# Performance work log

Hardware: AMD Instinct MI355X
Metric: run time of the kernel (lower is better)

The kernel has to match this reference:

```python
import jax, jax.numpy as jnp
from jax import lax
import numpy as np

STRIDE = 16
PRE_NMS = 100        # pre_nms_topN hardcoded in original forward
NMS_THRESH = 0.3
MIN_SIZE = 8.0


def _mk(ws, hs, xc, yc):
    return np.stack([xc - 0.5 * (ws - 1), yc - 0.5 * (hs - 1),
                     xc + 0.5 * (ws - 1), yc + 0.5 * (hs - 1)], axis=1)


def _generate_anchors(base_size=16, ratios=(0.5, 1.0, 2.0), scales=(8, 16, 32)):
    ratios = np.asarray(ratios, np.float64)
    scales = np.asarray(scales, np.float64)
    xc = yc = 0.5 * (base_size - 1)
    size = float(base_size) * float(base_size)
    ws = np.round(np.sqrt(size / ratios))
    hs = np.round(ws * ratios)
    ratio_anchors = _mk(ws, hs, xc, yc)
    out = []
    for a in ratio_anchors:
        aw = a[2] - a[0] + 1.0
        ah = a[3] - a[1] + 1.0
        axc = a[0] + 0.5 * (aw - 1)
        ayc = a[1] + 0.5 * (ah - 1)
        out.append(_mk(aw * scales, ah * scales, axc, ayc))
    return np.concatenate(out, axis=0)

ANCHORS = jnp.asarray(_generate_anchors(16, (0.5, 1.0, 2.0), (8, 16, 32)), jnp.float32)  # [9,4]
A = ANCHORS.shape[0]


def setup_inputs() -> dict:
    key = jax.random.key(0)
    k1, k2 = jax.random.split(key)
    B, H, W = 32, 80, 120
    score = jax.random.normal(k1, (B, 2 * A, H, W), jnp.float32)
    delta = jax.random.normal(k2, (B, 4 * A, H, W), jnp.float32)
    img = jnp.array([H * STRIDE, W * STRIDE, 1.0], jnp.float32)  # (im_h, im_w, scale)
    return {"score": score, "delta": delta, "img": img}


def _nms_one(bx, sv, vd):
    # bx: [P,4] boxes sorted by score, sv: [P] scores, vd: [P] valid mask
    b = lax.stop_gradient(bx)  # NMS selection is non-differentiable (index-based)
    x1, y1, x2, y2 = b[:, 0], b[:, 1], b[:, 2], b[:, 3]
    area = (x2 - x1 + 1.0) * (y2 - y1 + 1.0)
    iw = jnp.clip(jnp.minimum(x2[:, None], x2[None, :]) - jnp.maximum(x1[:, None], x1[None, :]) + 1.0, 0.0)
    ih = jnp.clip(jnp.minimum(y2[:, None], y2[None, :]) - jnp.maximum(y1[:, None], y1[None, :]) + 1.0, 0.0)
    inter = iw * ih
    iou = inter / (area[:, None] + area[None, :] - inter)  # [P,P]
    idx = jnp.arange(PRE_NMS)

    def body(i, keep):
        sup = (iou[i] > NMS_THRESH) & (idx > i) & keep[i]
        return keep & ~sup

    keep = lax.fori_loop(0, PRE_NMS, body, vd)
    # compact kept rows to the front, zeros after (matches original's zero-padded output)
    pos = jnp.cumsum(keep) - 1
    dst = jnp.where(keep, pos, PRE_NMS)  # dropped rows go to scratch row
    rows = jnp.concatenate([bx, sv[:, None]], axis=1)  # [P,5]
    return jnp.zeros((PRE_NMS + 1, 5), bx.dtype).at[dst].set(rows)[:PRE_NMS]


def reference(score, delta, img):
    B, _, h, w = delta.shape
    # objectness scores: second half of channels, laid out (h, w, A)
    scores = score[:, A:, :, :].transpose(0, 2, 3, 1).reshape(B, -1)  # [B, h*w*A]
    # shifts enumerated j over h (outer), i over w (inner)
    sx, sy = jnp.meshgrid(jnp.arange(w) * STRIDE, jnp.arange(h) * STRIDE)  # [h,w]
    shifts = jnp.stack([sx.ravel(), sy.ravel(), sx.ravel(), sy.ravel()], axis=1).astype(score.dtype)
    anchors = (ANCHORS[None, :, :] + shifts[:, None, :]).reshape(-1, 4)  # [h*w*A, 4]
    # NOTE: original assigns deltas = delta.view(B,-1,4), discarding the permute (bug kept)
    deltas = delta.reshape(B, -1, 4)
    # bbox_transform_inv
    aw = anchors[:, 2] - anchors[:, 0] + 1.0
    ah = anchors[:, 3] - anchors[:, 1] + 1.0
    acx = anchors[:, 0] + 0.5 * aw
    acy = anchors[:, 1] + 0.5 * ah
    pcx = deltas[:, :, 0] * aw + acx
    pcy = deltas[:, :, 1] * ah + acy
    pw = jnp.exp(deltas[:, :, 2]) * aw
    ph = jnp.exp(deltas[:, :, 3]) * ah
    x1 = pcx - 0.5 * pw
    y1 = pcy - 0.5 * ph
    x2 = pcx + 0.5 * pw
    y2 = pcy + 0.5 * ph
    # clip_boxes to image: x in [0, im_w-1], y in [0, im_h-1]
    x1 = jnp.clip(x1, 0.0, img[1] - 1.0)
    x2 = jnp.clip(x2, 0.0, img[1] - 1.0)
    y1 = jnp.clip(y1, 0.0, img[0] - 1.0)
    y2 = jnp.clip(y2, 0.0, img[0] - 1.0)
    proposals = jnp.stack([x1, y1, x2, y2], axis=-1)  # [B,N,4]
    # _filter_boxes with keep[0] applied to ALL images (bug in original, kept)
    ws_ = x2 - x1 + 1.0
    hs_ = y2 - y1 + 1.0
    keep0 = (ws_[0] >= MIN_SIZE) & (hs_[0] >= MIN_SIZE)  # [N]
    scores = jnp.where(keep0[None, :], scores, -jnp.inf)  # filtered boxes sort last
    topv, topi = lax.top_k(scores, PRE_NMS)  # [B,P]
    boxes = jnp.take_along_axis(proposals, topi[:, :, None], axis=1)  # [B,P,4]
    valid = jnp.isfinite(topv)
    return jax.vmap(_nms_one)(boxes, topv, valid)  # [B,P,5]
```

## Files before the change

### kernel.cpp

```cpp
#include <hip/hip_runtime.h>
#include <math.h>

#define NA     9
#define HH     80
#define WWID   120
#define HWSZ   (HH * WWID)
#define NANC   (HWSZ * NA)
#define NANC4  (NANC / 4)
#define PRE_NMS 100
#define NMS_THRESH 0.3f
#define MIN_SIZE 8.0f
#define STRIDE_F 16.0f
#define NCH    22
#define SLOTS  46
#define NFAST  (NCH * SLOTS)
#define NBIN   4096
#define CAPF   2048
#define T0ORD  0xC0300000u

__constant__ float c_aw[NA] = {184.f, 368.f, 736.f, 128.f, 256.f, 512.f,  88.f, 176.f, 352.f};
__constant__ float c_ah[NA] = { 96.f, 192.f, 384.f, 128.f, 256.f, 512.f, 176.f, 352.f, 704.f};

__device__ inline void decode_box(int n, float4 d, float imgW, float imgH,
                                  float& x1, float& y1, float& x2, float& y2) {
    int a = n % NA;
    int s = n / NA;
    int yy = s / WWID;
    int xx = s - yy * WWID;
    float aw = c_aw[a], ah = c_ah[a];
    float acx = 8.0f + STRIDE_F * (float)xx;
    float acy = 8.0f + STRIDE_F * (float)yy;
    float pcx = d.x * aw + acx;
    float pcy = d.y * ah + acy;
    float pw  = expf(d.z) * aw;
    float ph  = expf(d.w) * ah;
    x1 = pcx - 0.5f * pw;
    y1 = pcy - 0.5f * ph;
    x2 = pcx + 0.5f * pw;
    y2 = pcy + 0.5f * ph;
    float mx = imgW - 1.0f, my = imgH - 1.0f;
    x1 = fminf(fmaxf(x1, 0.0f), mx);
    x2 = fminf(fmaxf(x2, 0.0f), mx);
    y1 = fminf(fmaxf(y1, 0.0f), my);
    y2 = fminf(fmaxf(y2, 0.0f), my);
}

__device__ inline unsigned int f32_ord(float v) {
    unsigned int u = __float_as_uint(v);
    return (u & 0x80000000u) ? ~u : (u | 0x80000000u);
}
__device__ inline float ord_f32(unsigned int ov) {
    unsigned int u = (ov & 0x80000000u) ? (ov ^ 0x80000000u) : ~ov;
    return __uint_as_float(u);
}

__device__ inline bool keep_mask(int n, const float4* __restrict__ d0,
                                 float imgW, float imgH) {
    float x1, y1, x2, y2;
    decode_box(n, d0[n], imgW, imgH, x1, y1, x2, y2);
    return (x2 - x1 + 1.0f >= MIN_SIZE) && (y2 - y1 + 1.0f >= MIN_SIZE);
}

__global__ __launch_bounds__(256)
void k_compact(const float* __restrict__ score,
               const float* __restrict__ delta,
               const float* __restrict__ img,
               unsigned long long* __restrict__ cand,
               unsigned int* __restrict__ cnts) {
    __shared__ unsigned int lcnt;
    int chunk = blockIdx.x, b = blockIdx.y, tid = threadIdx.x;
    if (tid == 0) lcnt = 0u;
    __syncthreads();

    const float4* fg = reinterpret_cast<const float4*>(
        score + (size_t)b * (2 * NA * HWSZ) + (size_t)NA * HWSZ);
    const float4* d0 = reinterpret_cast<const float4*>(delta);
    float imgH = img[0], imgW = img[1];
    unsigned long long* myc = cand + ((size_t)b * NCH + chunk) * SLOTS;

    #pragma unroll
    for (int it = 0; it < 4; ++it) {
        int q = chunk * 1024 + it * 256 + tid;
        if (q < NANC4) {
            float4 v = fg[q];
            float vv[4] = {v.x, v.y, v.z, v.w};
            #pragma unroll
            for (int c = 0; c < 4; ++c) {
                unsigned ov = f32_ord(vv[c]);
                if (ov >= T0ORD) {
                    int m = 4 * q + c;
                    int a = m / HWSZ;
                    int s = m - a * HWSZ;
                    int n = s * NA + a;
                    if (keep_mask(n, d0, imgW, imgH)) {
                        unsigned slot = atomicAdd(&lcnt, 1u);
                        if (slot < SLOTS)
                            myc[slot] = ((unsigned long long)ov << 32) |
                                        (unsigned long long)(0xFFFFFFFFu - (unsigned)n);
                    }
                }
            }
        }
    }
    __syncthreads();
    unsigned cnt = lcnt;
    if (tid == 0) cnts[b * NCH + chunk] = cnt;
    for (unsigned l = cnt + tid; l < SLOTS; l += 256) myc[l] = 0ull;
}

__device__ inline void bitonic_desc(unsigned long long* sh, int S, int nthr) {
    for (int k = 2; k <= S; k <<= 1) {
        for (int j = k >> 1; j > 0; j >>= 1) {
            for (int i = threadIdx.x; i < S; i += nthr) {
                int ix = i ^ j;
                if (ix > i) {
                    unsigned long long va = sh[i], vb = sh[ix];
                    bool up = ((i & k) == 0);
                    bool sw = up ? (va < vb) : (va > vb);
                    if (sw) { sh[i] = vb; sh[ix] = va; }
                }
            }
            __syncthreads();
        }
    }
}

__global__ __launch_bounds__(256)
void k_final(const unsigned long long* __restrict__ cand,
             const unsigned int* __restrict__ cnts,
             const float* __restrict__ score,
             const float* __restrict__ delta,
             const float* __restrict__ img,
             float* __restrict__ out) {
    __shared__ unsigned long long sh[CAPF];
    __shared__ float bx1[PRE_NMS], by1[PRE_NMS], bx2[PRE_NMS], by2[PRE_NMS];
    __shared__ float bsc[PRE_NMS], barea[PRE_NMS];
    __shared__ unsigned int supW[PRE_NMS * 4];
    __shared__ unsigned int keepW[4];
    __shared__ int osrc[PRE_NMS];
    __shared__ unsigned int part[256];
    __shared__ int best;
    __shared__ unsigned int scnt;

    int b = blockIdx.x, tid = threadIdx.x;
    float imgH = img[0], imgW = img[1];
    const float4* fg = reinterpret_cast<const float4*>(
        score + (size_t)b * (2 * NA * HWSZ) + (size_t)NA * HWSZ);
    const float4* d0 = reinterpret_cast<const float4*>(delta);

    unsigned total = 0; bool over = false;
    for (int c = 0; c < NCH; ++c) {
        unsigned cc = cnts[b * NCH + c];
        total += cc;
        over = over || (cc > SLOTS);
    }
    bool fast = (!over) && (total >= PRE_NMS);

    int S;
    if (fast) {
        const unsigned long long* src = cand + (size_t)b * NFAST;
        for (int l = tid; l < 1024; l += 256)
            sh[l] = (l < NFAST) ? src[l] : 0ull;
        S = 1024;
    } else {
        unsigned int* lh = reinterpret_cast<unsigned int*>(sh);
        for (int i = tid; i < NBIN; i += 256) lh[i] = 0u;
        if (tid == 0) best = 0;
        __syncthreads();
        for (int q = tid; q < NANC4; q += 256) {
            float4 v = fg[q];
            float vv[4] = {v.x, v.y, v.z, v.w};
            #pragma unroll
            for (int c = 0; c < 4; ++c) {
                int m = 4 * q + c;
                int a = m / HWSZ;
                int s = m - a * HWSZ;
                int n = s * NA + a;
                float av = keep_mask(n, d0, imgW, imgH) ? vv[c] : -INFINITY;
                atomicAdd(&lh[f32_ord(av) >> 20], 1u);
            }
        }
        __syncthreads();
        unsigned g[16]; unsigned ssum = 0;
        #pragma unroll
        for (int j = 0; j < 16; ++j) { g[j] = lh[tid * 16 + j]; ssum += g[j]; }
        part[tid] = ssum;
        __syncthreads();
        for (int off = 1; off < 256; off <<= 1) {
            unsigned v = (tid + off < 256) ? part[tid + off] : 0u;
            __syncthreads();
            part[tid] += v;
            __syncthreads();
        }
        unsigned cum = (tid + 1 < 256) ? part[tid + 1] : 0u;
        int loc = -1;
        #pragma unroll
        for (int j = 15; j >= 0; --j) {
            cum += g[j];
            if (cum >= PRE_NMS) { loc = tid * 16 + j; break; }
        }
        if (loc >= 0) atomicMax(&best, loc);
        __syncthreads();
        unsigned T = (unsigned)best;
        if (tid == 0) scnt = 0u;
        for (int l = tid; l < CAPF; l += 256) sh[l] = 0ull;
        __syncthreads();
        for (int q = tid; q < NANC4; q += 256) {
            float4 v = fg[q];
            float vv[4] = {v.x, v.y, v.z, v.w};
            #pragma unroll
            for (int c = 0; c < 4; ++c) {
                int m = 4 * q + c;
                int a = m / HWSZ;
                int s = m - a * HWSZ;
                int n = s * NA + a;
                float av = keep_mask(n, d0, imgW, imgH) ? vv[c] : -INFINITY;
                unsigned ov = f32_ord(av);
                if ((ov >> 20) >= T) {
                    unsigned slot = atomicAdd(&scnt, 1u);
                    if (slot < CAPF)
                        sh[slot] = ((unsigned long long)ov << 32) |
                                   (unsigned long long)(0xFFFFFFFFu - (unsigned)n);
                }
            }
        }
        S = CAPF;
    }
    if (tid < 4) keepW[tid] = 0u;
    for (int i = tid; i < PRE_NMS * 4; i += 256) supW[i] = 0u;
    __syncthreads();

    bitonic_desc(sh, S, 256);

    if (tid < PRE_NMS) {
        unsigned long long key = sh[tid];
        float x1 = 0.f, y1 = 0.f, x2 = 0.f, y2 = 0.f, v = -INFINITY, ar = 1.f;
        if (key != 0ull) {
            unsigned n = 0xFFFFFFFFu - (unsigned)(key & 0xFFFFFFFFu);
            v = ord_f32((unsigned)(key >> 32));
            float4 d = reinterpret_cast<const float4*>(
                delta + (size_t)b * (4 * NANC))[n];
            decode_box((int)n, d, imgW, imgH, x1, y1, x2, y2);
            ar = (x2 - x1 + 1.0f) * (y2 - y1 + 1.0f);
        }
        bx1[tid] = x1; by1[tid] = y1; bx2[tid] = x2; by2[tid] = y2;
        bsc[tid] = v;  barea[tid] = ar;
        if (key != 0ull && isfinite(v))
            atomicOr(&keepW[tid >> 5], 1u << (tid & 31));
    }
    __syncthreads();

    for (int p = tid; p < PRE_NMS * PRE_NMS; p += 256) {
        int i = p / PRE_NMS;
        int j = p - i * PRE_NMS;
        if (j > i) {
            float ix1 = fmaxf(bx1[i], bx1[j]);
            float iy1 = fmaxf(by1[i], by1[j]);
            float ix2 = fminf(bx2[i], bx2[j]);
            float iy2 = fminf(by2[i], by2[j]);
            float iw = fmaxf(ix2 - ix1 + 1.0f, 0.0f);
            float ih = fmaxf(iy2 - iy1 + 1.0f, 0.0f);
            float inter = iw * ih;
            float iou = inter / (barea[i] + barea[j] - inter);
            if (iou > NMS_THRESH)
                atomicOr(&supW[i * 4 + (j >> 5)], 1u << (j & 31));
        }
    }
    __syncthreads();

    if (tid < 64) {
        unsigned r0w0 = supW[tid * 4 + 0], r0w1 = supW[tid * 4 + 1];
        unsigned r0w2 = supW[tid * 4 + 2], r0w3 = supW[tid * 4 + 3];
        unsigned r1w0 = 0, r1w1 = 0, r1w2 = 0, r1w3 = 0;
        if (tid < PRE_NMS - 64) {
            r1w0 = supW[(64 + tid) * 4 + 0]; r1w1 = supW[(64 + tid) * 4 + 1];
            r1w2 = supW[(64 + tid) * 4 + 2]; r1w3 = supW[(64 + tid) * 4 + 3];
        }
        unsigned kw0 = keepW[0], kw1 = keepW[1], kw2 = keepW[2], kw3 = keepW[3];
        #pragma unroll
        for (int i = 0; i < PRE_NMS - 1; ++i) {
            unsigned kword = (i < 32) ? kw0 : (i < 64) ? kw1 : (i < 96) ? kw2 : kw3;
            if ((kword >> (i & 31)) & 1u) {
                unsigned s0, s1, s2, s3;
                if (i < 64) {
                    s0 = __shfl(r0w0, i, 64); s1 = __shfl(r0w1, i, 64);
                    s2 = __shfl(r0w2, i, 64); s3 = __shfl(r0w3, i, 64);
                } else {
                    s0 = __shfl(r1w0, i - 64, 64); s1 = __shfl(r1w1, i - 64, 64);
                    s2 = __shfl(r1w2, i - 64, 64); s3 = __shfl(r1w3, i - 64, 64);
                }
                kw0 &= ~s0; kw1 &= ~s1; kw2 &= ~s2; kw3 &= ~s3;
            }
        }
        if (tid == 0) { keepW[0] = kw0; keepW[1] = kw1; keepW[2] = kw2; keepW[3] = kw3; }
    }
    __syncthreads();

    if (tid < PRE_NMS) osrc[tid] = -1;
    __syncthreads();
    if (tid < PRE_NMS) {
        unsigned k0 = keepW[0], k1 = keepW[1], k2 = keepW[2], k3 = keepW[3];
        int w = tid >> 5, bit = tid & 31;
        unsigned kword = (w == 0) ? k0 : (w == 1) ? k1 : (w == 2) ? k2 : k3;
        if ((kword >> bit) & 1u) {
            int pos = __popc(kword & ((1u << bit) - 1u));
            if (w > 0) pos += __popc(k0);
            if (w > 1) pos += __popc(k1);
            if (w > 2) pos += __popc(k2);
            osrc[pos] = tid;
        }
    }
    __syncthreads();

    float* ob = out + (size_t)b * (PRE_NMS * 5);
    if (tid < PRE_NMS) {
        int j = osrc[tid];
        float r0 = 0.f, r1 = 0.f, r2 = 0.f, r3 = 0.f, r4 = 0.f;
        if (j >= 0) { r0 = bx1[j]; r1 = by1[j]; r2 = bx2[j]; r3 = by2[j]; r4 = bsc[j]; }
        ob[tid * 5 + 0] = r0;
        ob[tid * 5 + 1] = r1;
        ob[tid * 5 + 2] = r2;
        ob[tid * 5 + 3] = r3;
        ob[tid * 5 + 4] = r4;
    }
}

extern "C" void kernel_launch(void* const* d_in, const int* in_sizes, int n_in,
                              void* d_out, int out_size, void* d_ws, size_t ws_size,
                              hipStream_t stream) {
    const float* score = (const float*)d_in[0];
    const float* delta = (const float*)d_in[1];
    const float* img   = (const float*)d_in[2];
    float* out = (float*)d_out;

    int B = in_sizes[0] / (2 * NA * HWSZ);

    unsigned long long* cand = (unsigned long long*)d_ws;
    unsigned int* cnts = (unsigned int*)((char*)d_ws +
                          (size_t)B * NCH * SLOTS * sizeof(unsigned long long));

    dim3 g1(NCH, B);
    k_compact<<<g1, 256, 0, stream>>>(score, delta, img, cand, cnts);
    k_final<<<B, 256, 0, stream>>>(cand, cnts, score, delta, img, out);
}
```

Before: 141.8 us.

## Compact candidates densely and sort a smaller power-of-two with 1024 threads

The final kernel now runs with 1024 threads per block instead of 256, and in the fast path it packs the per-chunk candidates contiguously using prefix sums of the chunk counts. It then sorts only the next power of two at or above the candidate total, with a minimum of 128, instead of a fixed 1024 entries. Both changes target the cost of the bitonic sort and its many barriers in a kernel launched with only B blocks. The price is larger blocks with more register pressure, and the slow path keeps only a quarter of the threads busy during the scan stages.

```diff
diff --git a/kernel.cpp b/kernel.cpp
--- a/kernel.cpp
+++ b/kernel.cpp
@@ -125,7 +125,7 @@
     }
 }
 
-__global__ __launch_bounds__(256)
+__global__ __launch_bounds__(1024)
 void k_final(const unsigned long long* __restrict__ cand,
              const unsigned int* __restrict__ cnts,
              const float* __restrict__ score,
@@ -133,6 +133,7 @@
              const float* __restrict__ img,
              float* __restrict__ out) {
     __shared__ unsigned long long sh[CAPF];
+    __shared__ unsigned int lcnts[NCH];
     __shared__ float bx1[PRE_NMS], by1[PRE_NMS], bx2[PRE_NMS], by2[PRE_NMS];
     __shared__ float bsc[PRE_NMS], barea[PRE_NMS];
     __shared__ unsigned int supW[PRE_NMS * 4];
@@ -148,9 +149,12 @@
         score + (size_t)b * (2 * NA * HWSZ) + (size_t)NA * HWSZ);
     const float4* d0 = reinterpret_cast<const float4*>(delta);
 
+    if (tid < NCH) lcnts[tid] = cnts[b * NCH + tid];
+    __syncthreads();
+
     unsigned total = 0; bool over = false;
     for (int c = 0; c < NCH; ++c) {
-        unsigned cc = cnts[b * NCH + c];
+        unsigned cc = lcnts[c];
         total += cc;
         over = over || (cc > SLOTS);
     }
@@ -158,16 +162,29 @@
 
     int S;
     if (fast) {
-        const unsigned long long* src = cand + (size_t)b * NFAST;
-        for (int l = tid; l < 1024; l += 256)
-            sh[l] = (l < NFAST) ? src[l] : 0ull;
-        S = 1024;
+        S = 128;
+        while (S < (int)total) S <<= 1;
+        for (int l = tid; l < S; l += 1024) sh[l] = 0ull;
+        __syncthreads();
+        if (tid < NFAST) {
+            int c  = tid / SLOTS;
+            int sl = tid - c * SLOTS;
+            unsigned cc = lcnts[c];
+            if ((unsigned)sl < cc) {
+                unsigned pre = 0;
+                #pragma unroll
+                for (int k2 = 0; k2 < NCH; ++k2)
+                    if (k2 < c) pre += lcnts[k2];
+                sh[pre + sl] = cand[((size_t)b * NCH + c) * SLOTS + sl];
+            }
+        }
+        __syncthreads();
     } else {
         unsigned int* lh = reinterpret_cast<unsigned int*>(sh);
-        for (int i = tid; i < NBIN; i += 256) lh[i] = 0u;
+        for (int i = tid; i < NBIN; i += 1024) lh[i] = 0u;
         if (tid == 0) best = 0;
         __syncthreads();
-        for (int q = tid; q < NANC4; q += 256) {
+        for (int q = tid; q < NANC4; q += 1024) {
             float4 v = fg[q];
             float vv[4] = {v.x, v.y, v.z, v.w};
             #pragma unroll
@@ -182,30 +199,36 @@
         }
         __syncthreads();
         unsigned g[16]; unsigned ssum = 0;
-        #pragma unroll
-        for (int j = 0; j < 16; ++j) { g[j] = lh[tid * 16 + j]; ssum += g[j]; }
-        part[tid] = ssum;
+        if (tid < 256) {
+            #pragma unroll
+            for (int j = 0; j < 16; ++j) { g[j] = lh[tid * 16 + j]; ssum += g[j]; }
+            part[tid] = ssum;
+        }
         __syncthreads();
         for (int off = 1; off < 256; off <<= 1) {
-            unsigned v = (tid + off < 256) ? part[tid + off] : 0u;
+            unsigned v = 0;
+            if (tid < 256 && tid + off < 256) v = part[tid + off];
             __syncthreads();
-            part[tid] += v;
+            if (tid < 256) part[tid] += v;
             __syncthreads();
         }
-        unsigned cum = (tid + 1 < 256) ? part[tid + 1] : 0u;
-        int loc = -1;
-        #pragma unroll
-        for (int j = 15; j >= 0; --j) {
-            cum += g[j];
-            if (cum >= PRE_NMS) { loc = tid * 16 + j; break; }
-        }
-        if (loc >= 0) atomicMax(&best, loc);
+        if (tid < 256) {
+            unsigned cum = (tid + 1 < 256) ? part[tid + 1] : 0u;
+            int loc = -1;
+            #pragma unroll
+            for (int j = 15; j >= 0; --j) {
+                cum += g[j];
+                if (cum >= PRE_NMS) { loc = tid * 16 + j; break; }
+            }
+            if (loc >= 0) atomicMax(&best, loc);
+        }
         __syncthreads();
         unsigned T = (unsigned)best;
         if (tid == 0) scnt = 0u;
-        for (int l = tid; l < CAPF; l += 256) sh[l] = 0ull;
-        __syncthreads();
-        for (int q = tid; q < NANC4; q += 256) {
+        __syncthreads();
+        for (int l = tid; l < CAPF; l += 1024) sh[l] = 0ull;
+        __syncthreads();
+        for (int q = tid; q < NANC4; q += 1024) {
             float4 v = fg[q];
             float vv[4] = {v.x, v.y, v.z, v.w};
             #pragma unroll
@@ -227,10 +250,10 @@
         S = CAPF;
     }
     if (tid < 4) keepW[tid] = 0u;
-    for (int i = tid; i < PRE_NMS * 4; i += 256) supW[i] = 0u;
-    __syncthreads();
-
-    bitonic_desc(sh, S, 256);
+    for (int i = tid; i < PRE_NMS * 4; i += 1024) supW[i] = 0u;
+    __syncthreads();
+
+    bitonic_desc(sh, S, 1024);
 
     if (tid < PRE_NMS) {
         unsigned long long key = sh[tid];
@@ -250,7 +273,7 @@
     }
     __syncthreads();
 
-    for (int p = tid; p < PRE_NMS * PRE_NMS; p += 256) {
+    for (int p = tid; p < PRE_NMS * PRE_NMS; p += 1024) {
         int i = p / PRE_NMS;
         int j = p - i * PRE_NMS;
         if (j > i) {
@@ -341,5 +364,5 @@
 
     dim3 g1(NCH, B);
     k_compact<<<g1, 256, 0, stream>>>(score, delta, img, cand, cnts);
-    k_final<<<B, 256, 0, stream>>>(cand, cnts, score, delta, img, out);
-}
+    k_final<<<B, 1024, 0, stream>>>(cand, cnts, score, delta, img, out);
+}
```

New measurement: 116.4 us. 17.9% less time.
